# Kernel optimization log

Hardware: AMD Instinct MI355X
Metric: run time of the kernel (lower is better)

## Reference

```python
import jax, jax.numpy as jnp
import numpy as np

WIN = (7, 7)          # window_size
NUM_HEADS = 16
DIM = 512
NW = 64               # number of distinct shift-masks (groups)
B_WIN = 4096          # total windows across the batch (divisible by NW)
S = WIN[0] * WIN[1]   # 49 tokens per window


def _relative_position_index(wh, ww):
    coords = np.stack(np.meshgrid(np.arange(wh), np.arange(ww), indexing='ij'))  # [2,wh,ww]
    flat = coords.reshape(2, -1)                                                  # [2,S]
    rel = flat[:, :, None] - flat[:, None, :]                                     # [2,S,S]
    rel = rel.transpose(1, 2, 0)
    rel[:, :, 0] += wh - 1
    rel[:, :, 1] += ww - 1
    rel[:, :, 0] *= 2 * ww - 1
    return rel.sum(-1).astype(np.int32)                                           # [S,S]


def setup_inputs() -> dict:
    key = jax.random.key(0)
    ks = jax.random.split(key, 6)
    x = jax.random.normal(ks[0], (B_WIN, S, DIM), dtype=jnp.float32)
    # Swin-style shift mask: 0 where tokens attend, -100 where masked.
    keep = jax.random.uniform(ks[1], (NW, S, S)) < 0.8
    mask = jnp.where(keep, 0.0, -100.0).astype(jnp.float32)
    Wqkv = jax.random.normal(ks[2], (DIM, 3 * DIM), dtype=jnp.float32) * 0.02
    bqkv = jnp.zeros((3 * DIM,), dtype=jnp.float32)
    Wproj = jax.random.normal(ks[3], (DIM, DIM), dtype=jnp.float32) * 0.02
    bproj = jnp.zeros((DIM,), dtype=jnp.float32)
    num_rel = (2 * WIN[0] - 1) * (2 * WIN[1] - 1)  # 169
    bias_table = jax.random.normal(ks[4], (num_rel, NUM_HEADS), dtype=jnp.float32) * 0.02
    rel_index = jnp.asarray(_relative_position_index(*WIN))  # [S,S] int32
    return {"x": x, "mask": mask, "Wqkv": Wqkv, "bqkv": bqkv,
            "Wproj": Wproj, "bproj": bproj, "bias_table": bias_table,
            "rel_index": rel_index}


def reference(x, mask, Wqkv, bqkv, Wproj, bproj, bias_table, rel_index):
    B_, S_, C = x.shape
    H = NUM_HEADS
    hd = C // H
    scale = hd ** -0.5
    qkv = (x @ Wqkv + bqkv).reshape(B_, S_, 3, H, hd).transpose(2, 0, 3, 1, 4)  # [3,B_,H,S,hd]
    q, k, v = qkv[0] * scale, qkv[1], qkv[2]
    attn = jnp.einsum('bhqd,bhkd->bhqk', q, k)  # [B_,H,S,S]
    # gathered relative position bias: [S,S,H] -> [H,S,S]
    bias = bias_table[rel_index.reshape(-1)].reshape(S_, S_, H).transpose(2, 0, 1)
    attn = attn + bias[None]
    nW = mask.shape[0]
    attn = attn.reshape(-1, nW, H, S_, S_) + mask[None, :, None]  # broadcast shift mask
    attn = jax.nn.softmax(attn.reshape(-1, H, S_, S_), axis=-1)
    out = jnp.einsum('bhqk,bhkd->bhqd', attn, v)
    out = out.transpose(0, 2, 1, 3).reshape(B_, S_, C)
    return out @ Wproj + bproj
```

## Files before the change

kernel.cpp:

```cpp
#include <hip/hip_runtime.h>


typedef short  v8s __attribute__((ext_vector_type(8)));
typedef float  v4f __attribute__((ext_vector_type(4)));

#define B_WIN 4096
#define S_TOK 49
#define DIM   512
#define NH    16
#define HD    32
#define NW    64
#define M_TOT (B_WIN * S_TOK)

__device__ __forceinline__ unsigned short f2bfu(float f) {
    unsigned u = __builtin_bit_cast(unsigned, f);
    u += 0x7fffu + ((u >> 16) & 1u);
    return (unsigned short)(u >> 16);
}


__global__ void cvt_x_kernel(const float4* __restrict__ x, ushort4* __restrict__ xb, int n4) {
    int i = blockIdx.x * 256 + threadIdx.x;
    if (i < n4) {
        float4 v = x[i];
        ushort4 o;
        o.x = f2bfu(v.x); o.y = f2bfu(v.y); o.z = f2bfu(v.z); o.w = f2bfu(v.w);
        xb[i] = o;
    }
}

__global__ void cvt_wt_kernel(const float* __restrict__ W, unsigned short* __restrict__ Wt,
                              int K, int N) {
    int idx = blockIdx.x * 256 + threadIdx.x;
    if (idx >= N * K) return;
    int n = idx / K, k = idx - n * K;
    Wt[idx] = f2bfu(W[(size_t)k * N + n]);
}

__global__ void build_bm_kernel(const float* __restrict__ bias_table,
                                const int* __restrict__ rel_index,
                                const float* __restrict__ mask,
                                float* __restrict__ bm) {
    int idx = blockIdx.x * 256 + threadIdx.x;
    int ij = idx % 2401;
    int gh = idx / 2401;
    int h = gh & 15, g = gh >> 4;
    bm[idx] = bias_table[rel_index[ij] * NH + h] + mask[g * 2401 + ij];
}

template <int OUT_BF16>
__global__ __launch_bounds__(256) void gemm_bt(
    const unsigned short* __restrict__ A,
    const unsigned short* __restrict__ Bt,
    const float* __restrict__ bias,
    void* __restrict__ Cout,
    int M, int N, int K) {
    __shared__ unsigned short As[128 * 32];
    __shared__ unsigned short Bs[128 * 32];
    const int tid  = threadIdx.x;
    const int wave = tid >> 6;
    const int lane = tid & 63;
    const int r    = lane & 15;
    const int quad = lane >> 4;
    const int m0 = blockIdx.y * 128;
    const int n0 = blockIdx.x * 128;
    const int woffm = (wave >> 1) * 64;
    const int woffn = (wave & 1) * 64;

    const char* gA = (const char*)(A + (size_t)m0 * K);
    const char* gB = (const char*)(Bt + (size_t)n0 * K);
    char* lA = (char*)As;
    char* lB = (char*)Bs;
    const int c0 = wave * 2;

    v4f acc[4][4] = {};

    for (int k0 = 0; k0 < K; k0 += 32) {
        __syncthreads();
#pragma unroll
        for (int hh = 0; hh < 2; ++hh) {
            int f   = (c0 + hh) * 1024 + lane * 16;
            int row = f >> 6;
            int kb  = f & 63;
            __builtin_amdgcn_global_load_lds(
                (const __attribute__((address_space(1))) unsigned int*)(gA + (size_t)row * (K * 2) + k0 * 2 + kb),
                (__attribute__((address_space(3))) unsigned int*)(lA + f), 16, 0, 0);
            __builtin_amdgcn_global_load_lds(
                (const __attribute__((address_space(1))) unsigned int*)(gB + (size_t)row * (K * 2) + k0 * 2 + kb),
                (__attribute__((address_space(3))) unsigned int*)(lB + f), 16, 0, 0);
        }
        __syncthreads();

        v8s af[4], bfr[4];
#pragma unroll
        for (int t = 0; t < 4; ++t)
            af[t] = *(const v8s*)(lA + ((woffm + 16 * t + r) * 32 + quad * 8) * 2);
#pragma unroll
        for (int t = 0; t < 4; ++t)
            bfr[t] = *(const v8s*)(lB + ((woffn + 16 * t + r) * 32 + quad * 8) * 2);
#pragma unroll
        for (int i = 0; i < 4; ++i)
#pragma unroll
            for (int j = 0; j < 4; ++j)
                acc[i][j] = __builtin_amdgcn_mfma_f32_16x16x32_bf16(af[i], bfr[j], acc[i][j], 0, 0, 0);
    }

#pragma unroll
    for (int j = 0; j < 4; ++j) {
        int n = n0 + woffn + 16 * j + r;
        float bv = bias[n];
#pragma unroll
        for (int i = 0; i < 4; ++i) {
#pragma unroll
            for (int rg = 0; rg < 4; ++rg) {
                int m = m0 + woffm + 16 * i + quad * 4 + rg;
                float val = acc[i][j][rg] + bv;
                if (OUT_BF16)
                    ((unsigned short*)Cout)[(size_t)m * N + n] = f2bfu(val);
                else
                    ((float*)Cout)[(size_t)m * N + n] = val;
            }
        }
    }
}

__global__ __launch_bounds__(256) void attn_kernel(
    const unsigned short* __restrict__ qkv,
    const float* __restrict__ bm,
    unsigned short* __restrict__ out) {
    const int w    = blockIdx.x;
    const int wave = threadIdx.x >> 6;
    const int h    = blockIdx.y * 4 + wave;
    const int lane = threadIdx.x & 63;
    const int r    = lane & 15;
    const int quad = lane >> 4;
    const int g    = w & (NW - 1);
    const size_t base = (size_t)w * S_TOK;

    __shared__ unsigned short pbuf[4][64 * 72];
    __shared__ unsigned short vbuf[4][32 * 72];
    unsigned short* p_lds = pbuf[wave];
    unsigned short* vt    = vbuf[wave];

    {
        int j = lane;
        union { uint4 q[4]; unsigned short s[32]; } vv;
        if (j < S_TOK) {
            const uint4* vrow = (const uint4*)(qkv + (base + j) * 1536 + 1024 + (size_t)h * HD);
#pragma unroll
            for (int c = 0; c < 4; ++c) vv.q[c] = vrow[c];
        } else {
#pragma unroll
            for (int c = 0; c < 4; ++c) vv.q[c] = make_uint4(0, 0, 0, 0);
        }
#pragma unroll
        for (int d = 0; d < HD; ++d) vt[d * 72 + j] = vv.s[d];
    }

    v8s zf = {0, 0, 0, 0, 0, 0, 0, 0};
    v8s aq[4], bk[4];
#pragma unroll
    for (int t = 0; t < 4; ++t) {
        int row = 16 * t + r;
        if (row < S_TOK) {
            const unsigned short* qp = qkv + (base + row) * 1536 + (size_t)h * HD + quad * 8;
            aq[t] = *(const v8s*)qp;
            bk[t] = *(const v8s*)(qp + 512);
        } else {
            aq[t] = zf;
            bk[t] = zf;
        }
    }

    v4f sc[4][4] = {};
#pragma unroll
    for (int i = 0; i < 4; ++i)
#pragma unroll
        for (int j = 0; j < 4; ++j)
            sc[i][j] = __builtin_amdgcn_mfma_f32_16x16x32_bf16(aq[i], bk[j], sc[i][j], 0, 0, 0);

    const float scale = 0.17677669529663687f;
    const float* bmh = bm + (size_t)(g * NH + h) * 2401;
#pragma unroll
    for (int it = 0; it < 4; ++it) {
#pragma unroll
        for (int rg = 0; rg < 4; ++rg) {
            int i = 16 * it + quad * 4 + rg;
            float s[4];
#pragma unroll
            for (int jt = 0; jt < 4; ++jt) {
                int j = 16 * jt + r;
                float v = sc[it][jt][rg] * scale;
                if (i < S_TOK && j < S_TOK) v += bmh[i * 49 + j];
                if (j >= S_TOK) v = -1e30f;
                s[jt] = v;
            }
            float mx = fmaxf(fmaxf(s[0], s[1]), fmaxf(s[2], s[3]));
#pragma unroll
            for (int d = 1; d < 16; d <<= 1) mx = fmaxf(mx, __shfl_xor(mx, d));
            float sum = 0.f;
#pragma unroll
            for (int jt = 0; jt < 4; ++jt) { s[jt] = __expf(s[jt] - mx); sum += s[jt]; }
#pragma unroll
            for (int d = 1; d < 16; d <<= 1) sum += __shfl_xor(sum, d);
            float inv = 1.0f / sum;
#pragma unroll
            for (int jt = 0; jt < 4; ++jt) sc[it][jt][rg] = s[jt] * inv;
        }
    }

#pragma unroll
    for (int it = 0; it < 4; ++it)
#pragma unroll
        for (int jt = 0; jt < 4; ++jt)
#pragma unroll
            for (int rg = 0; rg < 4; ++rg) {
                int i = 16 * it + quad * 4 + rg;
                int j = 16 * jt + r;
                p_lds[i * 72 + j] = f2bfu(sc[it][jt][rg]);
            }

    __syncthreads();

    v4f oacc[4][2] = {};
#pragma unroll
    for (int kt = 0; kt < 2; ++kt) {
        v8s bv[2];
#pragma unroll
        for (int nt = 0; nt < 2; ++nt)
            bv[nt] = *(const v8s*)(vt + (16 * nt + r) * 72 + 32 * kt + quad * 8);
#pragma unroll
        for (int it = 0; it < 4; ++it) {
            v8s ap = *(const v8s*)(p_lds + (16 * it + r) * 72 + 32 * kt + quad * 8);
#pragma unroll
            for (int nt = 0; nt < 2; ++nt)
                oacc[it][nt] = __builtin_amdgcn_mfma_f32_16x16x32_bf16(ap, bv[nt], oacc[it][nt], 0, 0, 0);
        }
    }

#pragma unroll
    for (int it = 0; it < 4; ++it)
#pragma unroll
        for (int nt = 0; nt < 2; ++nt)
#pragma unroll
            for (int rg = 0; rg < 4; ++rg) {
                int i = 16 * it + quad * 4 + rg;
                if (i < S_TOK)
                    out[(base + i) * DIM + h * HD + 16 * nt + r] = f2bfu(oacc[it][nt][rg]);
            }
}


extern "C" void kernel_launch(void* const* d_in, const int* in_sizes, int n_in,
                              void* d_out, int out_size, void* d_ws, size_t ws_size,
                              hipStream_t stream) {
    const float* x          = (const float*)d_in[0];
    const float* mask       = (const float*)d_in[1];
    const float* Wqkv       = (const float*)d_in[2];
    const float* bqkv       = (const float*)d_in[3];
    const float* Wproj      = (const float*)d_in[4];
    const float* bproj      = (const float*)d_in[5];
    const float* bias_table = (const float*)d_in[6];
    const int*   rel_index  = (const int*)d_in[7];
    float* out = (float*)d_out;

    char* ws = (char*)d_ws;
    unsigned short* qkv    = (unsigned short*)(ws);
    unsigned short* xbf    = (unsigned short*)(ws + 616562688);
    unsigned short* wqkvt  = (unsigned short*)(ws + 822083584);
    unsigned short* wprojt = (unsigned short*)(ws + 823656448);
    float*          bm     = (float*)(ws + 824180736);

    cvt_x_kernel<<<100352, 256, 0, stream>>>((const float4*)x, (ushort4*)xbf, 25690112);
    cvt_wt_kernel<<<(1536 * 512) / 256, 256, 0, stream>>>(Wqkv, wqkvt, 512, 1536);
    cvt_wt_kernel<<<(512 * 512) / 256, 256, 0, stream>>>(Wproj, wprojt, 512, 512);
    build_bm_kernel<<<(NW * NH * 2401) / 256, 256, 0, stream>>>(bias_table, rel_index, mask, bm);

    gemm_bt<1><<<dim3(12, 1568), 256, 0, stream>>>(xbf, wqkvt, bqkv, qkv, M_TOT, 1536, 512);

    attn_kernel<<<dim3(B_WIN, 4), 256, 0, stream>>>(qkv, bm, xbf);

    gemm_bt<0><<<dim3(4, 1568), 256, 0, stream>>>(xbf, wprojt, bproj, out, M_TOT, 512, 512);
}
```

Baseline: 1.829 ms.

## Replace GEMM with 256x256 double-buffered swizzled-LDS pipelined kernel

Replaces the 128x128 single-buffered GEMM with a 256x256-tile, 512-thread kernel. It double-buffers A/B in 128KB of LDS, uses an XOR-swizzled layout to avoid bank conflicts, and interleaves global-to-LDS loads with MFMA phases using barriers and setprio. Grid indices are remapped in chunks of 8 for better L2 locality. The aim is more data reuse per tile and less exposed load latency in both projection GEMMs. The cost is more complex synchronisation, hand-tuned vmcnt waits and heavy register and LDS pressure, which limits occupancy.

```diff
diff --git a/kernel.cpp b/kernel.cpp
--- a/kernel.cpp
+++ b/kernel.cpp
@@ -49,72 +49,167 @@
 }
 
 template <int OUT_BF16>
-__global__ __launch_bounds__(256) void gemm_bt(
+__global__ __launch_bounds__(512, 2) void gemm256(
     const unsigned short* __restrict__ A,
     const unsigned short* __restrict__ Bt,
     const float* __restrict__ bias,
     void* __restrict__ Cout,
     int M, int N, int K) {
-    __shared__ unsigned short As[128 * 32];
-    __shared__ unsigned short Bs[128 * 32];
+    __shared__ alignas(16) char lds[131072];
+    char* const As0 = lds;
+    char* const As1 = lds + 32768;
+    char* const Bs0 = lds + 65536;
+    char* const Bs1 = lds + 98304;
+
     const int tid  = threadIdx.x;
+    const int lane = tid & 63;
     const int wave = tid >> 6;
-    const int lane = tid & 63;
     const int r    = lane & 15;
-    const int quad = lane >> 4;
-    const int m0 = blockIdx.y * 128;
-    const int n0 = blockIdx.x * 128;
-    const int woffm = (wave >> 1) * 64;
-    const int woffn = (wave & 1) * 64;
-
-    const char* gA = (const char*)(A + (size_t)m0 * K);
-    const char* gB = (const char*)(Bt + (size_t)n0 * K);
-    char* lA = (char*)As;
-    char* lB = (char*)Bs;
-    const int c0 = wave * 2;
-
-    v4f acc[4][4] = {};
-
-    for (int k0 = 0; k0 < K; k0 += 32) {
-        __syncthreads();
-#pragma unroll
-        for (int hh = 0; hh < 2; ++hh) {
-            int f   = (c0 + hh) * 1024 + lane * 16;
-            int row = f >> 6;
-            int kb  = f & 63;
-            __builtin_amdgcn_global_load_lds(
-                (const __attribute__((address_space(1))) unsigned int*)(gA + (size_t)row * (K * 2) + k0 * 2 + kb),
-                (__attribute__((address_space(3))) unsigned int*)(lA + f), 16, 0, 0);
-            __builtin_amdgcn_global_load_lds(
-                (const __attribute__((address_space(1))) unsigned int*)(gB + (size_t)row * (K * 2) + k0 * 2 + kb),
-                (__attribute__((address_space(3))) unsigned int*)(lB + f), 16, 0, 0);
-        }
-        __syncthreads();
-
-        v8s af[4], bfr[4];
-#pragma unroll
-        for (int t = 0; t < 4; ++t)
-            af[t] = *(const v8s*)(lA + ((woffm + 16 * t + r) * 32 + quad * 8) * 2);
-#pragma unroll
-        for (int t = 0; t < 4; ++t)
-            bfr[t] = *(const v8s*)(lB + ((woffn + 16 * t + r) * 32 + quad * 8) * 2);
-#pragma unroll
-        for (int i = 0; i < 4; ++i)
-#pragma unroll
-            for (int j = 0; j < 4; ++j)
-                acc[i][j] = __builtin_amdgcn_mfma_f32_16x16x32_bf16(af[i], bfr[j], acc[i][j], 0, 0, 0);
-    }
-
-#pragma unroll
-    for (int j = 0; j < 4; ++j) {
-        int n = n0 + woffn + 16 * j + r;
-        float bv = bias[n];
-#pragma unroll
-        for (int i = 0; i < 4; ++i) {
+    const int q    = lane >> 4;
+    const int wr   = wave >> 2;
+    const int wc   = wave & 3;
+
+    const int nTx     = N >> 8;
+    const int chunk   = gridDim.x >> 3;
+    const int logical = (blockIdx.x & 7) * chunk + (blockIdx.x >> 3);
+    const int bx = logical % nTx;
+    const int by = logical / nTx;
+    const int m0 = by << 8;
+    const int n0 = bx << 8;
+
+    const int K2 = K << 1;
+
+    const int rs  = tid >> 3;
+    const int skS = ((tid & 7) ^ (rs & 7)) << 4;
+    const char* gAx = (const char*)(A  + (size_t)m0 * K) + (size_t)rs * K2 + skS;
+    const char* gBx = (const char*)(Bt + (size_t)n0 * K) + (size_t)rs * K2 + skS;
+
+#define STAGE(gsrc, ltile, hf, kt)                                               \
+    {                                                                            \
+        _Pragma("unroll")                                                        \
+        for (int l_ = 0; l_ < 2; ++l_) {                                         \
+            __builtin_amdgcn_global_load_lds(                                    \
+                (const __attribute__((address_space(1))) unsigned int*)(         \
+                    (gsrc) + (size_t)((hf) * 128 + l_ * 64) * K2 + (kt) * 128),  \
+                (__attribute__((address_space(3))) unsigned int*)(               \
+                    (ltile) + (hf) * 16384 + l_ * 8192 + tid * 16),              \
+                16, 0, 0);                                                       \
+        }                                                                        \
+    }
+
+    const int skb0 = ((q)     ^ (r & 7)) << 4;
+    const int skb1 = ((q + 4) ^ (r & 7)) << 4;
+    const int rowA = (wr * 128 + r) << 7;
+    const int rowB = (wc * 64  + r) << 7;
+
+#define RDA(tile, mi, ks) (*(const v8s*)((tile) + rowA + (mi) * 2048 + ((ks) ? skb1 : skb0)))
+#define RDB(tile, ni, ks) (*(const v8s*)((tile) + rowB + (ni) * 2048 + ((ks) ? skb1 : skb0)))
+
+    v4f acc[8][4] = {};
+    v8s fa[4][2];
+    v8s fb[4][2];
+
+#define MM(ah, bh)                                                                   \
+    {                                                                                \
+        __builtin_amdgcn_s_setprio(1);                                               \
+        _Pragma("unroll")                                                            \
+        for (int i_ = 0; i_ < 4; ++i_)                                               \
+            _Pragma("unroll")                                                        \
+            for (int j_ = 0; j_ < 2; ++j_)                                           \
+                _Pragma("unroll")                                                    \
+                for (int k_ = 0; k_ < 2; ++k_)                                       \
+                    acc[(ah) + i_][(bh) + j_] = __builtin_amdgcn_mfma_f32_16x16x32_bf16( \
+                        fa[i_][k_], fb[(bh) + j_][k_], acc[(ah) + i_][(bh) + j_], 0, 0, 0); \
+        __builtin_amdgcn_s_setprio(0);                                               \
+    }
+
+    const int NT     = K >> 6;
+    const int niters = NT >> 1;
+
+    STAGE(gBx, Bs0, 0, 0); STAGE(gBx, Bs0, 1, 0);
+    STAGE(gAx, As0, 0, 0); STAGE(gAx, As0, 1, 0);
+    STAGE(gBx, Bs1, 0, 1); STAGE(gBx, Bs1, 1, 1);
+    asm volatile("s_waitcnt vmcnt(4)" ::: "memory");
+    __builtin_amdgcn_s_barrier();
+
+    for (int i = 0; i < niters; ++i) {
+        const int t1 = 2 * i + 1;
+        const int t2 = 2 * i + 2;
+        const int t3 = 2 * i + 3;
+        const bool more = (i + 1) < niters;
+
+#pragma unroll
+        for (int mi = 0; mi < 4; ++mi) { fa[mi][0] = RDA(As0, mi, 0); fa[mi][1] = RDA(As0, mi, 1); }
+#pragma unroll
+        for (int ni = 0; ni < 2; ++ni) { fb[ni][0] = RDB(Bs0, ni, 0); fb[ni][1] = RDB(Bs0, ni, 1); }
+        STAGE(gAx, As1, 0, t1);
+        __builtin_amdgcn_s_barrier();
+        MM(0, 0);
+        __builtin_amdgcn_s_barrier();
+
+#pragma unroll
+        for (int ni = 2; ni < 4; ++ni) { fb[ni][0] = RDB(Bs0, ni, 0); fb[ni][1] = RDB(Bs0, ni, 1); }
+        STAGE(gAx, As1, 1, t1);
+        __builtin_amdgcn_s_barrier();
+        MM(0, 2);
+        __builtin_amdgcn_s_barrier();
+
+#pragma unroll
+        for (int mi = 0; mi < 4; ++mi) { fa[mi][0] = RDA(As0, mi + 4, 0); fa[mi][1] = RDA(As0, mi + 4, 1); }
+        if (more) STAGE(gBx, Bs0, 0, t2);
+        __builtin_amdgcn_s_barrier();
+        MM(4, 2);
+        __builtin_amdgcn_s_barrier();
+
+        if (more) STAGE(gBx, Bs0, 1, t2);
+        __builtin_amdgcn_s_barrier();
+        MM(4, 0);
+        if (more) { asm volatile("s_waitcnt vmcnt(4)" ::: "memory"); }
+        else      { asm volatile("s_waitcnt vmcnt(0)" ::: "memory"); }
+        __builtin_amdgcn_s_barrier();
+
+#pragma unroll
+        for (int mi = 0; mi < 4; ++mi) { fa[mi][0] = RDA(As1, mi, 0); fa[mi][1] = RDA(As1, mi, 1); }
+#pragma unroll
+        for (int ni = 0; ni < 2; ++ni) { fb[ni][0] = RDB(Bs1, ni, 0); fb[ni][1] = RDB(Bs1, ni, 1); }
+        if (more) STAGE(gAx, As0, 0, t2);
+        __builtin_amdgcn_s_barrier();
+        MM(0, 0);
+        __builtin_amdgcn_s_barrier();
+
+#pragma unroll
+        for (int ni = 2; ni < 4; ++ni) { fb[ni][0] = RDB(Bs1, ni, 0); fb[ni][1] = RDB(Bs1, ni, 1); }
+        if (more) STAGE(gAx, As0, 1, t2);
+        __builtin_amdgcn_s_barrier();
+        MM(0, 2);
+        __builtin_amdgcn_s_barrier();
+
+#pragma unroll
+        for (int mi = 0; mi < 4; ++mi) { fa[mi][0] = RDA(As1, mi + 4, 0); fa[mi][1] = RDA(As1, mi + 4, 1); }
+        if (more) STAGE(gBx, Bs1, 0, t3);
+        __builtin_amdgcn_s_barrier();
+        MM(4, 2);
+        __builtin_amdgcn_s_barrier();
+
+        if (more) STAGE(gBx, Bs1, 1, t3);
+        __builtin_amdgcn_s_barrier();
+        MM(4, 0);
+        if (more) { asm volatile("s_waitcnt vmcnt(4)" ::: "memory"); }
+        __builtin_amdgcn_s_barrier();
+    }
+
+    const int nb = n0 + wc * 64 + r;
+    const int mb = m0 + wr * 128 + q * 4;
+#pragma unroll
+    for (int ni = 0; ni < 4; ++ni) {
+        const int n = nb + ni * 16;
+        const float bv = bias[n];
+#pragma unroll
+        for (int mi = 0; mi < 8; ++mi) {
 #pragma unroll
             for (int rg = 0; rg < 4; ++rg) {
-                int m = m0 + woffm + 16 * i + quad * 4 + rg;
-                float val = acc[i][j][rg] + bv;
+                const int m = mb + mi * 16 + rg;
+                float val = acc[mi][ni][rg] + bv;
                 if (OUT_BF16)
                     ((unsigned short*)Cout)[(size_t)m * N + n] = f2bfu(val);
                 else
@@ -122,6 +217,10 @@
             }
         }
     }
+#undef STAGE
+#undef RDA
+#undef RDB
+#undef MM
 }
 
 __global__ __launch_bounds__(256) void attn_kernel(
@@ -276,9 +375,9 @@
     cvt_wt_kernel<<<(512 * 512) / 256, 256, 0, stream>>>(Wproj, wprojt, 512, 512);
     build_bm_kernel<<<(NW * NH * 2401) / 256, 256, 0, stream>>>(bias_table, rel_index, mask, bm);
 
-    gemm_bt<1><<<dim3(12, 1568), 256, 0, stream>>>(xbf, wqkvt, bqkv, qkv, M_TOT, 1536, 512);
+    gemm256<1><<<dim3(4704), 512, 0, stream>>>(xbf, wqkvt, bqkv, qkv, M_TOT, 1536, 512);
 
     attn_kernel<<<dim3(B_WIN, 4), 256, 0, stream>>>(qkv, bm, xbf);
 
-    gemm_bt<0><<<dim3(4, 1568), 256, 0, stream>>>(xbf, wprojt, bproj, out, M_TOT, 512, 512);
-}
+    gemm256<0><<<dim3(1568), 512, 0, stream>>>(xbf, wprojt, bproj, out, M_TOT, 512, 512);
+}
```

New measurement: 1.636 ms. 10.5% less time.
